# Kernel tuning notes

Measured on AMD Instinct MI355X. Metric: run time of the kernel, lower is better.

Reference implementation:

```python
import jax, jax.numpy as jnp
import numpy as np

B, N, D = 4, 4096, 256

def setup_inputs() -> dict:
    key = jax.random.key(0)
    k1, = jax.random.split(key, 1)
    x = jax.random.normal(k1, (B, N, D), dtype=jnp.float32)
    attn_mask = jnp.ones((B, 1, N), dtype=jnp.int32)
    pad_mask = jnp.ones((B, 1, N), dtype=jnp.int32)
    return {"x": x, "attn_mask": attn_mask, "pad_mask": pad_mask, "dim_": D}

def reference(x, attn_mask, pad_mask, dim_):
    # adj is None -> scores = x @ x^T / sqrt(d)
    scale = jnp.sqrt(jnp.asarray(x.shape[-1], x.dtype))
    scores = jnp.einsum('bnd,bmd->bnm', x, x) / scale  # [B, N, N]
    # NOTE: original calls non-in-place masked_fill and discards the result,
    # so pad_mask / attn_mask have no effect on the output (faithful).
    prob = jax.nn.softmax(scores, axis=-1)
    # dropout is identity in inference mode
    return jnp.einsum('bnm,bmd->bnd', prob, x)
```

## Files before the change

kernel.cpp:

```cpp
#include <hip/hip_runtime.h>

typedef __attribute__((ext_vector_type(8))) short short8;
typedef __attribute__((ext_vector_type(4))) float f32x4;
typedef __attribute__((ext_vector_type(4))) unsigned int u32x4;

#define NTOK 4096
#define DIM  256
#define P_STRIDE 72
#define TILE_ELEMS 32768

__device__ __forceinline__ unsigned pack2bf(float a, float b) {
  unsigned ua = __builtin_bit_cast(unsigned, a) + 0x8000u;
  unsigned ub = __builtin_bit_cast(unsigned, b) + 0x8000u;
  return __builtin_amdgcn_perm(ub, ua, 0x07060302u);
}

__global__ __launch_bounds__(256, 4)
void prep_kernel(const float* __restrict__ X, unsigned short* __restrict__ Img) {
  const int b    = blockIdx.x & 3;
  const int sub  = blockIdx.x >> 2;
  const int t    = sub >> 3;
  const int part = sub & 7;
  const int tid  = threadIdx.x;
  const float* src = X + ((size_t)b * NTOK + t * 64) * DIM;
  unsigned short* dst = Img + ((size_t)(b * 64 + t)) * TILE_ELEMS;
  {
    int r = part * 8 + (tid >> 5);
    int c = tid & 31;
    const float* s = src + r * DIM + c * 8;
    f32x4 f0 = *(const f32x4*)s;
    f32x4 f1 = *(const f32x4*)(s + 4);
    union { unsigned u[4]; u32x4 v; } p;
    p.u[0] = pack2bf(f0[0], f0[1]);
    p.u[1] = pack2bf(f0[2], f0[3]);
    p.u[2] = pack2bf(f1[0], f1[1]);
    p.u[3] = pack2bf(f1[2], f1[3]);
    *(u32x4*)(dst + r * 256 + ((c ^ (r & 7)) << 3)) = p.v;
  }
  {
    const int d = tid;
    float f[8];
    #pragma unroll
    for (int i = 0; i < 8; ++i) f[i] = src[(part * 8 + i) * DIM + d];
    union { unsigned u[4]; u32x4 v; } p;
    p.u[0] = pack2bf(f[0], f[1]);
    p.u[1] = pack2bf(f[2], f[3]);
    p.u[2] = pack2bf(f[4], f[5]);
    p.u[3] = pack2bf(f[6], f[7]);
    *(u32x4*)(dst + 16384 + part * 2048 + d * 8) = p.v;
  }
}

__device__ __forceinline__ void pv_step(const unsigned short* __restrict__ pr,
                                        const unsigned short* __restrict__ kt,
                                        f32x4 (&o)[2][4],
                                        int qh, int role, int quad, int ln) {
  #pragma unroll
  for (int ks = 0; ks < 2; ++ks) {
    const int pos = (ks * 4 + quad) ^ ((ln >> 3) << 1);
    short8 ap[2], bv[4];
    #pragma unroll
    for (int s = 0; s < 2; ++s) {
      const int r = qh * 32 + s * 16 + ln;
      ap[s] = *(const short8*)(&pr[r * P_STRIDE + (pos << 3)]);
    }
    const unsigned short* kb = kt + (ks * 4 + quad) * 2048 + (role * 64 + ln) * 8;
    #pragma unroll
    for (int dt = 0; dt < 4; ++dt) bv[dt] = *(const short8*)(kb + dt * 128);
    #pragma unroll
    for (int s = 0; s < 2; ++s)
      #pragma unroll
      for (int dt = 0; dt < 4; ++dt)
        o[s][dt] = __builtin_amdgcn_mfma_f32_16x16x32_bf16(ap[s], bv[dt], o[s][dt], 0, 0, 0);
  }
}

__global__ __launch_bounds__(512, 1)
void fa_kernel(const unsigned short* __restrict__ Img, float* __restrict__ Out) {
  __shared__ __align__(16) unsigned short ksb[2][16384];
  __shared__ __align__(16) unsigned short ktb[2][16384];
  __shared__ __align__(16) unsigned short pb[2][64 * P_STRIDE];
  __shared__ float lbuf[64][4];

  const int tid  = threadIdx.x;
  const int b    = blockIdx.x & 3;
  const int qblk = blockIdx.x >> 2;
  const int wave = tid >> 6;
  const int lane = tid & 63;
  const int ln   = lane & 15;
  const int quad = lane >> 4;
  const int swz  = ln & 7;
  const int qh   = wave & 1;
  const int role = wave >> 1;

  const unsigned short* imgb  = Img + (size_t)b * 64 * TILE_ELEMS;
  const char*           imgbc = (const char*)imgb;

  short8 aQ[2][8];
  #pragma unroll
  for (int s = 0; s < 2; ++s) {
    const unsigned short* qrow =
        imgb + (size_t)qblk * TILE_ELEMS + (qh * 32 + s * 16 + ln) * 256;
    #pragma unroll
    for (int ds = 0; ds < 8; ++ds)
      aQ[s][ds] = *(const short8*)(qrow + (((ds * 4 + quad) ^ swz) << 3));
  }

  f32x4 o[2][4];
  #pragma unroll
  for (int s = 0; s < 2; ++s)
    #pragma unroll
    for (int dt = 0; dt < 4; ++dt) o[s][dt] = (f32x4)(0.0f);
  float lrow[2][4] = {{0.f,0.f,0.f,0.f},{0.f,0.f,0.f,0.f}};

  const float c2 = 0.0901684400f;

  const int pwPos = ((role * 2 + (ln >> 3)) ^ ((quad >> 1) << 1)) << 3;
  const int pwCol = ln & 7;

  const bool dmaKs = wave < 4;
  const int  dmaQ  = wave & 3;
  const char* gK = imgbc + (size_t)dmaQ * 8192 + (size_t)lane * 16;

  if (dmaKs) {
    #pragma unroll
    for (int i = 0; i < 8; ++i)
      __builtin_amdgcn_global_load_lds(
          (const __attribute__((address_space(1))) unsigned*)(gK + i * 1024),
          (__attribute__((address_space(3))) unsigned*)(&ksb[0][dmaQ * 4096 + i * 512]),
          16, 0, 0);
  }

  for (int t = 0; t < 64; ++t) {
    __syncthreads();
    const int buf = t & 1;

    if (dmaKs) {
      if (t < 63) {
        const char* g = gK + (size_t)(t + 1) * 65536;
        unsigned short* l = &ksb[buf ^ 1][dmaQ * 4096];
        #pragma unroll
        for (int i = 0; i < 8; ++i)
          __builtin_amdgcn_global_load_lds(
              (const __attribute__((address_space(1))) unsigned*)(g + i * 1024),
              (__attribute__((address_space(3))) unsigned*)(l + i * 512),
              16, 0, 0);
      }
    } else {
      const char* g = gK + (size_t)t * 65536 + 32768;
      unsigned short* l = &ktb[buf][dmaQ * 4096];
      #pragma unroll
      for (int i = 0; i < 8; ++i)
        __builtin_amdgcn_global_load_lds(
            (const __attribute__((address_space(1))) unsigned*)(g + i * 1024),
            (__attribute__((address_space(3))) unsigned*)(l + i * 512),
            16, 0, 0);
    }

    f32x4 sf0 = (f32x4)(0.0f), sf1 = (f32x4)(0.0f);
    {
      const unsigned short* krow = &ksb[buf][(role * 16 + ln) * 256];
      #pragma unroll
      for (int ds = 0; ds < 8; ++ds) {
        short8 bk = *(const short8*)(krow + (((ds * 4 + quad) ^ swz) << 3));
        sf0 = __builtin_amdgcn_mfma_f32_16x16x32_bf16(aQ[0][ds], bk, sf0, 0, 0, 0);
        sf1 = __builtin_amdgcn_mfma_f32_16x16x32_bf16(aQ[1][ds], bk, sf1, 0, 0, 0);
      }
    }
    {
      unsigned short* pw = pb[buf];
      #pragma unroll
      for (int j = 0; j < 4; ++j) {
        float p0 = __builtin_amdgcn_exp2f(sf0[j] * c2);
        float p1 = __builtin_amdgcn_exp2f(sf1[j] * c2);
        lrow[0][j] += p0;
        lrow[1][j] += p1;
        unsigned q0 = __builtin_bit_cast(unsigned, p0);
        unsigned q1 = __builtin_bit_cast(unsigned, p1);
        unsigned n0 = (unsigned)__builtin_amdgcn_mov_dpp((int)q0, 0xB1, 0xF, 0xF, true);
        unsigned n1 = (unsigned)__builtin_amdgcn_mov_dpp((int)q1, 0xB1, 0xF, 0xF, true);
        if ((ln & 1) == 0) {
          const int r0 = qh * 32 + quad * 4 + j;
          unsigned d0 = pack2bf(__builtin_bit_cast(float, q0), __builtin_bit_cast(float, n0));
          unsigned d1 = pack2bf(__builtin_bit_cast(float, q1), __builtin_bit_cast(float, n1));
          *(unsigned*)(&pw[r0 * P_STRIDE + pwPos + pwCol]) = d0;
          *(unsigned*)(&pw[(r0 + 16) * P_STRIDE + pwPos + pwCol]) = d1;
        }
      }
    }

    if (t > 0)
      pv_step(pb[buf ^ 1], ktb[buf ^ 1], o, qh, role, quad, ln);
  }

  __syncthreads();
  pv_step(pb[1], ktb[1], o, qh, role, quad, ln);

  #pragma unroll
  for (int off = 1; off < 16; off <<= 1)
    #pragma unroll
    for (int s = 0; s < 2; ++s)
      #pragma unroll
      for (int j = 0; j < 4; ++j)
        lrow[s][j] += __shfl_xor(lrow[s][j], off, 64);
  if (ln == 0) {
    #pragma unroll
    for (int s = 0; s < 2; ++s)
      #pragma unroll
      for (int j = 0; j < 4; ++j)
        lbuf[qh * 32 + s * 16 + quad * 4 + j][role] = lrow[s][j];
  }
  __syncthreads();

  #pragma unroll
  for (int s = 0; s < 2; ++s) {
    float* outp = Out + (size_t)(b * NTOK + qblk * 64 + qh * 32 + s * 16) * DIM + role * 64;
    #pragma unroll
    for (int j = 0; j < 4; ++j) {
      const int row = s * 16 + quad * 4 + j;
      f32x4 lv = *(const f32x4*)lbuf[qh * 32 + row];
      const float rl = 1.0f / (lv[0] + lv[1] + lv[2] + lv[3]);
      #pragma unroll
      for (int dt = 0; dt < 4; ++dt)
        outp[(size_t)(quad * 4 + j) * DIM + dt * 16 + ln] = o[s][dt][j] * rl;
    }
  }
}

extern "C" void kernel_launch(void* const* d_in, const int* in_sizes, int n_in,
                              void* d_out, int out_size, void* d_ws, size_t ws_size,
                              hipStream_t stream) {
  const float* X = (const float*)d_in[0];
  float* Out = (float*)d_out;
  unsigned short* Img = (unsigned short*)d_ws;
  (void)in_sizes; (void)n_in; (void)out_size; (void)ws_size;
  hipLaunchKernelGGL(prep_kernel, dim3(2048), dim3(256), 0, stream, X, Img);
  hipLaunchKernelGGL(fa_kernel, dim3(256), dim3(512), 0, stream, Img, Out);
}
```

Before: 173.7 us.

## Halve query tile to 32 rows and stream V from global into registers

The attention kernel now processes 32 query rows per block instead of 64, which doubles the grid to 512 blocks, and raises the launch-bounds occupancy hint. The V tile is no longer staged through LDS by dedicated DMA waves. Each wave loads its V fragment straight from global memory into registers, one iteration ahead. All 8 waves now share the K prefetch, and each wave covers a 32-dim slice of the output. This is meant to cut LDS usage so that more blocks fit per CU and to improve latency hiding. The cost is that every block re-reads the full K/V stream twice as often overall, which adds L2 traffic and exposes the per-thread global V loads.

```diff
diff --git a/kernel.cpp b/kernel.cpp
--- a/kernel.cpp
+++ b/kernel.cpp
@@ -51,40 +51,16 @@
   }
 }
 
-__device__ __forceinline__ void pv_step(const unsigned short* __restrict__ pr,
-                                        const unsigned short* __restrict__ kt,
-                                        f32x4 (&o)[2][4],
-                                        int qh, int role, int quad, int ln) {
-  #pragma unroll
-  for (int ks = 0; ks < 2; ++ks) {
-    const int pos = (ks * 4 + quad) ^ ((ln >> 3) << 1);
-    short8 ap[2], bv[4];
-    #pragma unroll
-    for (int s = 0; s < 2; ++s) {
-      const int r = qh * 32 + s * 16 + ln;
-      ap[s] = *(const short8*)(&pr[r * P_STRIDE + (pos << 3)]);
-    }
-    const unsigned short* kb = kt + (ks * 4 + quad) * 2048 + (role * 64 + ln) * 8;
-    #pragma unroll
-    for (int dt = 0; dt < 4; ++dt) bv[dt] = *(const short8*)(kb + dt * 128);
-    #pragma unroll
-    for (int s = 0; s < 2; ++s)
-      #pragma unroll
-      for (int dt = 0; dt < 4; ++dt)
-        o[s][dt] = __builtin_amdgcn_mfma_f32_16x16x32_bf16(ap[s], bv[dt], o[s][dt], 0, 0, 0);
-  }
-}
-
-__global__ __launch_bounds__(512, 1)
+__global__ __launch_bounds__(512, 4)
 void fa_kernel(const unsigned short* __restrict__ Img, float* __restrict__ Out) {
   __shared__ __align__(16) unsigned short ksb[2][16384];
-  __shared__ __align__(16) unsigned short ktb[2][16384];
-  __shared__ __align__(16) unsigned short pb[2][64 * P_STRIDE];
-  __shared__ float lbuf[64][4];
+  __shared__ __align__(16) unsigned short pb[2][32 * P_STRIDE];
+  __shared__ __align__(16) float lbuf[32][4];
 
   const int tid  = threadIdx.x;
-  const int b    = blockIdx.x & 3;
-  const int qblk = blockIdx.x >> 2;
+  const int bid  = blockIdx.x;
+  const int b    = (bid & 7) >> 1;
+  const int qblk = ((bid >> 3) << 1) | (bid & 1);
   const int wave = tid >> 6;
   const int lane = tid & 63;
   const int ln   = lane & 15;
@@ -96,133 +72,154 @@
   const unsigned short* imgb  = Img + (size_t)b * 64 * TILE_ELEMS;
   const char*           imgbc = (const char*)imgb;
 
-  short8 aQ[2][8];
-  #pragma unroll
-  for (int s = 0; s < 2; ++s) {
+  short8 aQ[8];
+  {
     const unsigned short* qrow =
-        imgb + (size_t)qblk * TILE_ELEMS + (qh * 32 + s * 16 + ln) * 256;
+        imgb + (size_t)(qblk >> 1) * TILE_ELEMS + ((qblk & 1) * 32 + qh * 16 + ln) * 256;
     #pragma unroll
     for (int ds = 0; ds < 8; ++ds)
-      aQ[s][ds] = *(const short8*)(qrow + (((ds * 4 + quad) ^ swz) << 3));
-  }
-
-  f32x4 o[2][4];
+      aQ[ds] = *(const short8*)(qrow + (((ds * 4 + quad) ^ swz) << 3));
+  }
+
+  f32x4 o[2][2];
   #pragma unroll
   for (int s = 0; s < 2; ++s)
     #pragma unroll
-    for (int dt = 0; dt < 4; ++dt) o[s][dt] = (f32x4)(0.0f);
-  float lrow[2][4] = {{0.f,0.f,0.f,0.f},{0.f,0.f,0.f,0.f}};
+    for (int dt = 0; dt < 2; ++dt) o[s][dt] = (f32x4)(0.0f);
+  float lrow[4] = {0.f, 0.f, 0.f, 0.f};
 
   const float c2 = 0.0901684400f;
 
   const int pwPos = ((role * 2 + (ln >> 3)) ^ ((quad >> 1) << 1)) << 3;
   const int pwCol = ln & 7;
 
-  const bool dmaKs = wave < 4;
-  const int  dmaQ  = wave & 3;
-  const char* gK = imgbc + (size_t)dmaQ * 8192 + (size_t)lane * 16;
-
-  if (dmaKs) {
-    #pragma unroll
-    for (int i = 0; i < 8; ++i)
-      __builtin_amdgcn_global_load_lds(
-          (const __attribute__((address_space(1))) unsigned*)(gK + i * 1024),
-          (__attribute__((address_space(3))) unsigned*)(&ksb[0][dmaQ * 4096 + i * 512]),
-          16, 0, 0);
-  }
+  const char* gK = imgbc + (size_t)wave * 4096 + (size_t)lane * 16;
+  #pragma unroll
+  for (int i = 0; i < 4; ++i)
+    __builtin_amdgcn_global_load_lds(
+        (const __attribute__((address_space(1))) unsigned*)(gK + i * 1024),
+        (__attribute__((address_space(3))) unsigned*)(&ksb[0][wave * 2048 + i * 512]),
+        16, 0, 0);
+
+  const unsigned short* ktbase = imgb + 16384 + (size_t)quad * 2048 + (wave * 32 + ln) * 8;
+
+  short8 bvA[2][2];
+  short8 bvN[2][2];
 
   for (int t = 0; t < 64; ++t) {
     __syncthreads();
     const int buf = t & 1;
 
-    if (dmaKs) {
-      if (t < 63) {
-        const char* g = gK + (size_t)(t + 1) * 65536;
-        unsigned short* l = &ksb[buf ^ 1][dmaQ * 4096];
-        #pragma unroll
-        for (int i = 0; i < 8; ++i)
-          __builtin_amdgcn_global_load_lds(
-              (const __attribute__((address_space(1))) unsigned*)(g + i * 1024),
-              (__attribute__((address_space(3))) unsigned*)(l + i * 512),
-              16, 0, 0);
-      }
-    } else {
-      const char* g = gK + (size_t)t * 65536 + 32768;
-      unsigned short* l = &ktb[buf][dmaQ * 4096];
-      #pragma unroll
-      for (int i = 0; i < 8; ++i)
+    if (t < 63) {
+      const char* g = gK + (size_t)(t + 1) * 65536;
+      unsigned short* l = &ksb[buf ^ 1][wave * 2048];
+      #pragma unroll
+      for (int i = 0; i < 4; ++i)
         __builtin_amdgcn_global_load_lds(
             (const __attribute__((address_space(1))) unsigned*)(g + i * 1024),
             (__attribute__((address_space(3))) unsigned*)(l + i * 512),
             16, 0, 0);
     }
 
-    f32x4 sf0 = (f32x4)(0.0f), sf1 = (f32x4)(0.0f);
+    {
+      const unsigned short* kt = ktbase + (size_t)t * TILE_ELEMS;
+      #pragma unroll
+      for (int ks = 0; ks < 2; ++ks)
+        #pragma unroll
+        for (int dt = 0; dt < 2; ++dt)
+          bvN[ks][dt] = *(const short8*)(kt + ks * 8192 + dt * 128);
+    }
+
+    f32x4 sf = (f32x4)(0.0f);
     {
       const unsigned short* krow = &ksb[buf][(role * 16 + ln) * 256];
       #pragma unroll
       for (int ds = 0; ds < 8; ++ds) {
         short8 bk = *(const short8*)(krow + (((ds * 4 + quad) ^ swz) << 3));
-        sf0 = __builtin_amdgcn_mfma_f32_16x16x32_bf16(aQ[0][ds], bk, sf0, 0, 0, 0);
-        sf1 = __builtin_amdgcn_mfma_f32_16x16x32_bf16(aQ[1][ds], bk, sf1, 0, 0, 0);
+        sf = __builtin_amdgcn_mfma_f32_16x16x32_bf16(aQ[ds], bk, sf, 0, 0, 0);
       }
     }
+
     {
       unsigned short* pw = pb[buf];
       #pragma unroll
       for (int j = 0; j < 4; ++j) {
-        float p0 = __builtin_amdgcn_exp2f(sf0[j] * c2);
-        float p1 = __builtin_amdgcn_exp2f(sf1[j] * c2);
-        lrow[0][j] += p0;
-        lrow[1][j] += p1;
+        float p0 = __builtin_amdgcn_exp2f(sf[j] * c2);
+        lrow[j] += p0;
         unsigned q0 = __builtin_bit_cast(unsigned, p0);
-        unsigned q1 = __builtin_bit_cast(unsigned, p1);
         unsigned n0 = (unsigned)__builtin_amdgcn_mov_dpp((int)q0, 0xB1, 0xF, 0xF, true);
-        unsigned n1 = (unsigned)__builtin_amdgcn_mov_dpp((int)q1, 0xB1, 0xF, 0xF, true);
         if ((ln & 1) == 0) {
-          const int r0 = qh * 32 + quad * 4 + j;
+          const int r0 = qh * 16 + quad * 4 + j;
           unsigned d0 = pack2bf(__builtin_bit_cast(float, q0), __builtin_bit_cast(float, n0));
-          unsigned d1 = pack2bf(__builtin_bit_cast(float, q1), __builtin_bit_cast(float, n1));
           *(unsigned*)(&pw[r0 * P_STRIDE + pwPos + pwCol]) = d0;
-          *(unsigned*)(&pw[(r0 + 16) * P_STRIDE + pwPos + pwCol]) = d1;
         }
       }
     }
 
-    if (t > 0)
-      pv_step(pb[buf ^ 1], ktb[buf ^ 1], o, qh, role, quad, ln);
+    if (t > 0) {
+      const unsigned short* pr = pb[buf ^ 1];
+      #pragma unroll
+      for (int ks = 0; ks < 2; ++ks) {
+        const int pos = (ks * 4 + quad) ^ ((ln >> 3) << 1);
+        short8 ap[2];
+        #pragma unroll
+        for (int s = 0; s < 2; ++s)
+          ap[s] = *(const short8*)(&pr[(s * 16 + ln) * P_STRIDE + (pos << 3)]);
+        #pragma unroll
+        for (int s = 0; s < 2; ++s)
+          #pragma unroll
+          for (int dt = 0; dt < 2; ++dt)
+            o[s][dt] = __builtin_amdgcn_mfma_f32_16x16x32_bf16(ap[s], bvA[ks][dt], o[s][dt], 0, 0, 0);
+      }
+    }
+
+    #pragma unroll
+    for (int ks = 0; ks < 2; ++ks)
+      #pragma unroll
+      for (int dt = 0; dt < 2; ++dt) bvA[ks][dt] = bvN[ks][dt];
   }
 
   __syncthreads();
-  pv_step(pb[1], ktb[1], o, qh, role, quad, ln);
+  {
+    const unsigned short* pr = pb[1];
+    #pragma unroll
+    for (int ks = 0; ks < 2; ++ks) {
+      const int pos = (ks * 4 + quad) ^ ((ln >> 3) << 1);
+      short8 ap[2];
+      #pragma unroll
+      for (int s = 0; s < 2; ++s)
+        ap[s] = *(const short8*)(&pr[(s * 16 + ln) * P_STRIDE + (pos << 3)]);
+      #pragma unroll
+      for (int s = 0; s < 2; ++s)
+        #pragma unroll
+        for (int dt = 0; dt < 2; ++dt)
+          o[s][dt] = __builtin_amdgcn_mfma_f32_16x16x32_bf16(ap[s], bvA[ks][dt], o[s][dt], 0, 0, 0);
+    }
+  }
 
   #pragma unroll
   for (int off = 1; off < 16; off <<= 1)
     #pragma unroll
-    for (int s = 0; s < 2; ++s)
-      #pragma unroll
-      for (int j = 0; j < 4; ++j)
-        lrow[s][j] += __shfl_xor(lrow[s][j], off, 64);
+    for (int j = 0; j < 4; ++j)
+      lrow[j] += __shfl_xor(lrow[j], off, 64);
   if (ln == 0) {
     #pragma unroll
-    for (int s = 0; s < 2; ++s)
-      #pragma unroll
-      for (int j = 0; j < 4; ++j)
-        lbuf[qh * 32 + s * 16 + quad * 4 + j][role] = lrow[s][j];
+    for (int j = 0; j < 4; ++j)
+      lbuf[qh * 16 + quad * 4 + j][role] = lrow[j];
   }
   __syncthreads();
 
   #pragma unroll
   for (int s = 0; s < 2; ++s) {
-    float* outp = Out + (size_t)(b * NTOK + qblk * 64 + qh * 32 + s * 16) * DIM + role * 64;
+    float* outp = Out + (size_t)(b * NTOK + qblk * 32 + s * 16) * DIM + wave * 32;
     #pragma unroll
     for (int j = 0; j < 4; ++j) {
-      const int row = s * 16 + quad * 4 + j;
-      f32x4 lv = *(const f32x4*)lbuf[qh * 32 + row];
+      const int row = quad * 4 + j;
+      f32x4 lv = *(const f32x4*)lbuf[s * 16 + row];
       const float rl = 1.0f / (lv[0] + lv[1] + lv[2] + lv[3]);
       #pragma unroll
-      for (int dt = 0; dt < 4; ++dt)
-        outp[(size_t)(quad * 4 + j) * DIM + dt * 16 + ln] = o[s][dt][j] * rl;
+      for (int dt = 0; dt < 2; ++dt)
+        outp[(size_t)row * DIM + dt * 16 + ln] = o[s][dt][j] * rl;
     }
   }
 }
@@ -235,5 +232,5 @@
   unsigned short* Img = (unsigned short*)d_ws;
   (void)in_sizes; (void)n_in; (void)out_size; (void)ws_size;
   hipLaunchKernelGGL(prep_kernel, dim3(2048), dim3(256), 0, stream, X, Img);
-  hipLaunchKernelGGL(fa_kernel, dim3(256), dim3(512), 0, stream, Img, Out);
-}
+  hipLaunchKernelGGL(fa_kernel, dim3(512), dim3(512), 0, stream, Img, Out);
+}
```

After: 182.5 us. 1.05x slower.
